# Performance work log

Measured on AMD Instinct MI355X. Metric: run time of the kernel, lower is better.

The kernel has to match this reference:

```python
import jax, jax.numpy as jnp
import numpy as np

EMBED = 1024
HEADS = 16
HEAD_DIM = EMBED // HEADS

def setup_inputs() -> dict:
    key = jax.random.key(0)
    ks = jax.random.split(key, 12)
    N, L, E = 4, 2048, EMBED
    s = 1.0 / np.sqrt(E)
    return {
        "values": jax.random.normal(ks[0], (N, L, E), jnp.float32),
        "keys": jax.random.normal(ks[1], (N, L, E), jnp.float32),
        "query": jax.random.normal(ks[2], (N, L, E), jnp.float32),
        "mask": jnp.ones((N, 1, 1, L), jnp.int32),
        "Wv": jax.random.normal(ks[3], (E, E), jnp.float32) * s,
        "bv": jnp.zeros((E,), jnp.float32),
        "Wk": jax.random.normal(ks[4], (E, E), jnp.float32) * s,
        "bk": jnp.zeros((E,), jnp.float32),
        "Wq": jax.random.normal(ks[5], (E, E), jnp.float32) * s,
        "bq": jnp.zeros((E,), jnp.float32),
        "Wo": jax.random.normal(ks[6], (E, E), jnp.float32) * s,
        "bo": jnp.zeros((E,), jnp.float32),
    }

def reference(values, keys, query, mask, Wv, bv, Wk, bk, Wq, bq, Wo, bo):
    N, L, E = values.shape
    H, D = HEADS, HEAD_DIM
    v = (values @ Wv + bv).reshape(N, L, H, D)
    k = (keys @ Wk + bk).reshape(N, L, H, D)
    q = (query @ Wq + bq).reshape(N, L, H, D)
    # energy: [N, H, Lq, Lk]
    energy = jnp.einsum('nqhd,nkhd->nhqk', q, k)
    energy = jnp.where(mask == 0, jnp.float32(-1e20), energy)
    attn = jax.nn.softmax(energy / np.sqrt(D), axis=3)
    out = jnp.einsum('nhqk,nkhd->nqhd', attn, v).reshape(N, L, E)
    return out @ Wo + bo
```

## Files before the change

### kernel.cpp

```cpp
#include <hip/hip_runtime.h>
#include <hip/hip_bf16.h>


#define N_B 4
#define L_S 2048
#define E_D 1024
#define H_N 16
#define D_H 64

typedef __attribute__((ext_vector_type(8))) short short8;
typedef __attribute__((ext_vector_type(8))) unsigned short ushort8;
typedef __attribute__((ext_vector_type(4))) unsigned short ushort4v;
typedef __attribute__((ext_vector_type(4))) float f32x4;

#define EXP2F(x) __builtin_amdgcn_exp2f(x)

__device__ __forceinline__ unsigned short f2b(float f) {
    unsigned int u = __builtin_bit_cast(unsigned int, f);
    u += 0x7fffu + ((u >> 16) & 1u);
    return (unsigned short)(u >> 16);
}

__device__ __forceinline__ void gload16(const void* g, void* l) {
    __builtin_amdgcn_global_load_lds(
        (const __attribute__((address_space(1))) void*)g,
        (__attribute__((address_space(3))) void*)l, 16, 0, 0);
}

__global__ __launch_bounds__(256) void cvt3_kernel(const float* __restrict__ v,
                                                   const float* __restrict__ k,
                                                   const float* __restrict__ q,
                                                   unsigned short* __restrict__ out) {
    int z = blockIdx.y;
    const float* in = (z == 0) ? v : ((z == 1) ? k : q);
    unsigned short* o = out + (size_t)z * (8u << 20);
    size_t i = (size_t)blockIdx.x * 256 + threadIdx.x;
    const float* p = in + i * 8;
    ushort8 ov;
#pragma unroll
    for (int j = 0; j < 8; j++) ov[j] = f2b(p[j]);
    *(ushort8*)(o + i * 8) = ov;
}

__global__ __launch_bounds__(256) void wtrans4_kernel(const float* __restrict__ W0,
                                                      const float* __restrict__ W1,
                                                      const float* __restrict__ W2,
                                                      const float* __restrict__ W3,
                                                      unsigned short* __restrict__ WtBase) {
    __shared__ float t[64][65];
    int z = blockIdx.z;
    const float* W = (z == 0) ? W0 : ((z == 1) ? W1 : ((z == 2) ? W2 : W3));
    unsigned short* Wt = WtBase + (size_t)z * (1u << 20);
    int bx = blockIdx.x, by = blockIdx.y;
    int tx = threadIdx.x;
    int r0 = tx >> 4;
    int c4 = (tx & 15) << 2;
#pragma unroll
    for (int rr = 0; rr < 64; rr += 16) {
        const float* src = W + (size_t)(by * 64 + rr + r0) * E_D + bx * 64 + c4;
        float4 v = *(const float4*)src;
        t[rr + r0][c4 + 0] = v.x; t[rr + r0][c4 + 1] = v.y;
        t[rr + r0][c4 + 2] = v.z; t[rr + r0][c4 + 3] = v.w;
    }
    __syncthreads();
#pragma unroll
    for (int rr = 0; rr < 64; rr += 16) {
        int nrow = bx * 64 + rr + r0;
        ushort4v o;
#pragma unroll
        for (int j = 0; j < 4; j++) o[j] = f2b(t[c4 + j][rr + r0]);
        *(ushort4v*)(Wt + (size_t)nrow * E_D + by * 64 + c4) = o;
    }
}

template <int OUTF32>
__device__ __forceinline__ void gemm_body(
    const unsigned short* __restrict__ A, const unsigned short* __restrict__ Bt,
    const float* __restrict__ bias, void* __restrict__ C,
    int K, int Nc, float scale,
    unsigned short* As, unsigned short* Bs, int n0, int m0) {
    int lane = threadIdx.x & 63, wave = threadIdx.x >> 6;
    int wr = (wave >> 1) * 64, wc = (wave & 1) * 64;
    f32x4 acc[4][4] = {};
    int nk = K >> 6;
    for (int kt = 0; kt < nk; ++kt) {
#pragma unroll
        for (int i = 0; i < 4; i++) {
            int c = (i * 4 + wave) * 64 + lane;
            int row = c >> 3;
            int csw = (c & 7) ^ (row & 7);
            gload16(A + (size_t)(m0 + row) * K + kt * 64 + csw * 8,
                    As + (size_t)(i * 4 + wave) * 512);
            gload16(Bt + (size_t)(n0 + row) * K + kt * 64 + csw * 8,
                    Bs + (size_t)(i * 4 + wave) * 512);
        }
        __syncthreads();
#pragma unroll
        for (int ks = 0; ks < 2; ++ks) {
            short8 a[4], b[4];
#pragma unroll
            for (int mi = 0; mi < 4; mi++) {
                int row = wr + mi * 16 + (lane & 15);
                int ch = (ks * 4 + (lane >> 4)) ^ (row & 7);
                a[mi] = *(const short8*)(As + row * 64 + ch * 8);
            }
#pragma unroll
            for (int ni = 0; ni < 4; ni++) {
                int col = wc + ni * 16 + (lane & 15);
                int ch = (ks * 4 + (lane >> 4)) ^ (col & 7);
                b[ni] = *(const short8*)(Bs + col * 64 + ch * 8);
            }
#pragma unroll
            for (int mi = 0; mi < 4; mi++)
#pragma unroll
                for (int ni = 0; ni < 4; ni++)
                    acc[mi][ni] = __builtin_amdgcn_mfma_f32_16x16x32_bf16(
                        a[mi], b[ni], acc[mi][ni], 0, 0, 0);
        }
        __syncthreads();
    }
#pragma unroll
    for (int ni = 0; ni < 4; ni++) {
        int col = n0 + wc + ni * 16 + (lane & 15);
        float bb = bias[col];
#pragma unroll
        for (int mi = 0; mi < 4; mi++) {
            int rbase = m0 + wr + mi * 16 + (lane >> 4) * 4;
#pragma unroll
            for (int r = 0; r < 4; r++) {
                float v = (acc[mi][ni][r] + bb) * scale;
                if (OUTF32)
                    ((float*)C)[(size_t)(rbase + r) * Nc + col] = v;
                else
                    ((unsigned short*)C)[(size_t)(rbase + r) * Nc + col] = f2b(v);
            }
        }
    }
}

template <int OUTF32>
__global__ __launch_bounds__(256, 3) void gemm_kernel(
    const unsigned short* __restrict__ A, const unsigned short* __restrict__ Bt,
    const float* __restrict__ bias, void* __restrict__ C,
    int M, int K, int Nc, float scale) {
    __shared__ unsigned short As[128 * 64];
    __shared__ unsigned short Bs[128 * 64];
    gemm_body<OUTF32>(A, Bt, bias, C, K, Nc, scale, As, Bs,
                      blockIdx.x * 128, blockIdx.y * 128);
}

__global__ __launch_bounds__(256, 3) void gemm3_kernel(
    const unsigned short* __restrict__ Abase, const unsigned short* __restrict__ Wtbase,
    const float* __restrict__ bv, const float* __restrict__ bk, const float* __restrict__ bq,
    unsigned short* __restrict__ Cbase, float qscale) {
    __shared__ unsigned short As[128 * 64];
    __shared__ unsigned short Bs[128 * 64];
    int z = blockIdx.z;
    const unsigned short* A  = Abase + (size_t)z * (8u << 20);
    const unsigned short* Bt = Wtbase + (size_t)z * (1u << 20);
    const float* bias = (z == 0) ? bv : ((z == 1) ? bk : bq);
    unsigned short* C = Cbase + (size_t)z * (8u << 20);
    float scale = (z == 2) ? qscale : 1.0f;
    gemm_body<0>(A, Bt, bias, C, E_D, E_D, scale, As, Bs,
                 blockIdx.x * 128, blockIdx.y * 128);
}

__global__ __launch_bounds__(256) void vtrans_kernel(const unsigned short* __restrict__ v,
                                                     unsigned short* __restrict__ vt) {
    __shared__ unsigned short t[64 * 65];
    int l0 = blockIdx.x * 64, h = blockIdx.y, n = blockIdx.z;
    int tx = threadIdx.x;
    int r = tx >> 3;
    int c8 = (tx & 7) << 3;
#pragma unroll
    for (int rr = 0; rr < 64; rr += 32) {
        ushort8 val = *(const ushort8*)(v + (size_t)(n * L_S + l0 + rr + r) * E_D + h * 64 + c8);
#pragma unroll
        for (int j = 0; j < 8; j++) t[(rr + r) * 65 + c8 + j] = val[j];
    }
    __syncthreads();
#pragma unroll
    for (int rr = 0; rr < 64; rr += 32) {
        int d = rr + r;
        ushort8 o;
#pragma unroll
        for (int j = 0; j < 8; j++) o[j] = t[(c8 + j) * 65 + d];
        *(ushort8*)(vt + (size_t)((n * H_N + h) * D_H + d) * L_S + l0 + c8) = o;
    }
}

__global__ __launch_bounds__(256, 3) void attn_kernel(
    const unsigned short* __restrict__ qb, const unsigned short* __restrict__ kb,
    const unsigned short* __restrict__ vt, const int* __restrict__ mask,
    unsigned short* __restrict__ aout) {
    __shared__ unsigned short Ks[2][64 * 64];
    __shared__ unsigned short Vs[2][64 * 64];
    __shared__ unsigned short Ps[4][32 * 64];
    __shared__ alignas(8) unsigned char okb[256];
    int lane = threadIdx.x & 63, wave = threadIdx.x >> 6;
    int g = lane >> 4, c = lane & 15;
    const float SHIFT = 20.0f;

    int bid = blockIdx.x;
    int w = (bid & 7) * 128 + (bid >> 3);
    int q0 = (w & 15) * 128;
    int h = (w >> 4) & 15;
    int n = w >> 8;

    const unsigned short* qptr  = qb + (size_t)n * L_S * E_D + h * 64;
    const unsigned short* kbase = kb + (size_t)n * L_S * E_D + h * 64;
    const unsigned short* vbase = vt + (size_t)(n * H_N + h) * D_H * L_S;
    const int* mbase = mask + n * L_S;

    {
        int t8 = threadIdx.x * 8;
        int4 ma = *(const int4*)(mbase + t8);
        int4 mb = *(const int4*)(mbase + t8 + 4);
        int ok = (ma.x != 0) & (ma.y != 0) & (ma.z != 0) & (ma.w != 0) &
                 (mb.x != 0) & (mb.y != 0) & (mb.z != 0) & (mb.w != 0);
        okb[threadIdx.x] = (unsigned char)ok;
    }
    unsigned short* Qs = &Ps[0][0];
#pragma unroll
    for (int i = 0; i < 4; i++) {
        int cc = (i * 4 + wave) * 64 + lane;
        int row = cc >> 3, csw = (cc & 7) ^ (row & 7);
        gload16(qptr + (size_t)(q0 + row) * E_D + csw * 8, Qs + (i * 4 + wave) * 512);
    }
#pragma unroll
    for (int i = 0; i < 2; i++) {
        int cc = (i * 4 + wave) * 64 + lane;
        int row = cc >> 3, csw = (cc & 7) ^ (row & 7);
        gload16(kbase + (size_t)row * E_D + csw * 8, Ks[0] + (i * 4 + wave) * 512);
        gload16(vbase + (size_t)row * L_S + csw * 8, Vs[0] + (i * 4 + wave) * 512);
    }
    __syncthreads();

    short8 qf[2][2];
#pragma unroll
    for (int m = 0; m < 2; m++)
#pragma unroll
        for (int kd = 0; kd < 2; kd++) {
            int row = wave * 32 + m * 16 + c;
            int ch = (kd * 4 + g) ^ (row & 7);
            qf[m][kd] = *(const short8*)(Qs + row * 64 + ch * 8);
        }

    f32x4 o[2][4] = {};
    float lrun[2] = {0.f, 0.f};
    unsigned short* pw = &Ps[wave][0];

    const int NT = L_S / 64;
    for (int kt = 0; kt < NT; ++kt) {
        int cur = kt & 1;
        if (kt + 1 < NT) {
#pragma unroll
            for (int i = 0; i < 2; i++) {
                int cc = (i * 4 + wave) * 64 + lane;
                int row = cc >> 3, csw = (cc & 7) ^ (row & 7);
                gload16(kbase + (size_t)((kt + 1) * 64 + row) * E_D + csw * 8,
                        Ks[cur ^ 1] + (i * 4 + wave) * 512);
                gload16(vbase + (size_t)row * L_S + (kt + 1) * 64 + csw * 8,
                        Vs[cur ^ 1] + (i * 4 + wave) * 512);
            }
            asm volatile("s_waitcnt vmcnt(4)" ::: "memory");
        } else {
            asm volatile("s_waitcnt vmcnt(0)" ::: "memory");
        }
        __builtin_amdgcn_s_barrier();
        __builtin_amdgcn_sched_barrier(0);

        const unsigned short* KsC = Ks[cur];
        const unsigned short* VsC = Vs[cur];

        f32x4 sT[2][4] = {};
        __builtin_amdgcn_s_setprio(1);
#pragma unroll
        for (int kd = 0; kd < 2; kd++)
#pragma unroll
            for (int kg = 0; kg < 4; kg++) {
                int krow = kg * 16 + c;
                int ch = (kd * 4 + g) ^ (krow & 7);
                short8 kf = *(const short8*)(KsC + krow * 64 + ch * 8);
                sT[0][kg] = __builtin_amdgcn_mfma_f32_16x16x32_bf16(kf, qf[0][kd], sT[0][kg], 0, 0, 0);
                sT[1][kg] = __builtin_amdgcn_mfma_f32_16x16x32_bf16(kf, qf[1][kd], sT[1][kg], 0, 0, 0);
            }
        __builtin_amdgcn_s_setprio(0);

        uint2 fl = *(const uint2*)&okb[kt * 8];
        bool dense = ((fl.x & fl.y) == 0x01010101u);
        if (!dense) {
#pragma unroll
            for (int kg = 0; kg < 4; kg++) {
                int4 mv = *(const int4*)(mbase + kt * 64 + kg * 16 + g * 4);
                float m0 = mv.x ? 0.f : -1e30f;
                float m1 = mv.y ? 0.f : -1e30f;
                float m2 = mv.z ? 0.f : -1e30f;
                float m3 = mv.w ? 0.f : -1e30f;
                sT[0][kg][0] += m0; sT[1][kg][0] += m0;
                sT[0][kg][1] += m1; sT[1][kg][1] += m1;
                sT[0][kg][2] += m2; sT[1][kg][2] += m2;
                sT[0][kg][3] += m3; sT[1][kg][3] += m3;
            }
        }
#pragma unroll
        for (int m = 0; m < 2; m++) {
            float ps = 0.f;
            int prow = m * 16 + c;
#pragma unroll
            for (int kg = 0; kg < 4; kg++) {
                float p0 = EXP2F(sT[m][kg][0] - SHIFT);
                float p1 = EXP2F(sT[m][kg][1] - SHIFT);
                float p2 = EXP2F(sT[m][kg][2] - SHIFT);
                float p3 = EXP2F(sT[m][kg][3] - SHIFT);
                ps += (p0 + p1) + (p2 + p3);
                unsigned int w0, w1;
                asm("v_cvt_pk_bf16_f32 %0, %1, %2" : "=v"(w0) : "v"(p0), "v"(p1));
                asm("v_cvt_pk_bf16_f32 %0, %1, %2" : "=v"(w1) : "v"(p2), "v"(p3));
                int c16 = kg * 2 + (g >> 1);
                int off = prow * 64 + ((c16 ^ (prow & 7)) << 3) + ((g & 1) << 2);
                uint2 wv; wv.x = w0; wv.y = w1;
                *(uint2*)(pw + off) = wv;
            }
            ps += __shfl_xor(ps, 16);
            ps += __shfl_xor(ps, 32);
            lrun[m] += ps;
        }
        __builtin_amdgcn_s_setprio(1);
#pragma unroll
        for (int kk = 0; kk < 2; kk++) {
            short8 pb[2];
#pragma unroll
            for (int m = 0; m < 2; m++) {
                int prow = m * 16 + c;
                int ch = (kk * 4 + g) ^ (prow & 7);
                pb[m] = *(const short8*)(pw + prow * 64 + ch * 8);
            }
#pragma unroll
            for (int dg = 0; dg < 4; dg++) {
                int drow = dg * 16 + c;
                int ch = (kk * 4 + g) ^ (drow & 7);
                short8 vb = *(const short8*)(VsC + drow * 64 + ch * 8);
                o[0][dg] = __builtin_amdgcn_mfma_f32_16x16x32_bf16(vb, pb[0], o[0][dg], 0, 0, 0);
                o[1][dg] = __builtin_amdgcn_mfma_f32_16x16x32_bf16(vb, pb[1], o[1][dg], 0, 0, 0);
            }
        }
        __builtin_amdgcn_s_setprio(0);
        asm volatile("s_waitcnt lgkmcnt(0)" ::: "memory");
        __builtin_amdgcn_s_barrier();
    }
#pragma unroll
    for (int m = 0; m < 2; m++) {
        float inv = 1.f / lrun[m];
        int row = q0 + wave * 32 + m * 16 + c;
#pragma unroll
        for (int dg = 0; dg < 4; dg++) {
            ushort4v ov;
#pragma unroll
            for (int r = 0; r < 4; r++) ov[r] = f2b(o[m][dg][r] * inv);
            *(ushort4v*)(aout + (size_t)(n * L_S + row) * E_D + h * 64 + dg * 16 + g * 4) = ov;
        }
    }
}

extern "C" void kernel_launch(void* const* d_in, const int* in_sizes, int n_in,
                              void* d_out, int out_size, void* d_ws, size_t ws_size,
                              hipStream_t stream) {
    const float* values = (const float*)d_in[0];
    const float* keys   = (const float*)d_in[1];
    const float* query  = (const float*)d_in[2];
    const int*   mask   = (const int*)d_in[3];
    const float* Wv = (const float*)d_in[4];  const float* bv = (const float*)d_in[5];
    const float* Wk = (const float*)d_in[6];  const float* bk = (const float*)d_in[7];
    const float* Wq = (const float*)d_in[8];  const float* bq = (const float*)d_in[9];
    const float* Wo = (const float*)d_in[10]; const float* bo = (const float*)d_in[11];
    float* out = (float*)d_out;
    char* ws = (char*)d_ws;
    const size_t MB = 1ull << 20;
    unsigned short* xv  = (unsigned short*)(ws + 0 * MB);
    unsigned short* wtv = (unsigned short*)(ws + 48 * MB);
    unsigned short* wto = (unsigned short*)(ws + 54 * MB);
    unsigned short* vbf = (unsigned short*)(ws + 56 * MB);
    unsigned short* kbf = (unsigned short*)(ws + 72 * MB);
    unsigned short* qbf = (unsigned short*)(ws + 88 * MB);
    unsigned short* vT  = (unsigned short*)(ws + 0 * MB);
    unsigned short* aob = (unsigned short*)(ws + 16 * MB);

    const float QS = 0.125f * 1.4426950408889634f;

    cvt3_kernel<<<dim3(4096, 3), 256, 0, stream>>>(values, keys, query, xv);
    wtrans4_kernel<<<dim3(16, 16, 4), 256, 0, stream>>>(Wv, Wk, Wq, Wo, wtv);
    gemm3_kernel<<<dim3(E_D / 128, (N_B * L_S) / 128, 3), 256, 0, stream>>>(
        xv, wtv, bv, bk, bq, vbf, QS);
    vtrans_kernel<<<dim3(32, 16, 4), 256, 0, stream>>>(vbf, vT);
    attn_kernel<<<dim3(1024), 256, 0, stream>>>(qbf, kbf, vT, mask, aob);
    gemm_kernel<1><<<dim3(E_D / 128, (N_B * L_S) / 128), 256, 0, stream>>>(
        aob, wto, bo, out, N_B * L_S, E_D, E_D, 1.0f);
}
```

Baseline: 229.9 us.

## Double attention query tile to 256 rows with 8 waves sharing K/V tiles

The attention kernel now launches 512 blocks of 512 threads. Each block handles 256 query rows with eight waves, so every K/V tile loaded into LDS is reused by twice as many query rows and total K/V traffic is halved. The block-to-(batch, head, query-tile) mapping is rearranged so that blocks sharing a head land on the same XCD. The costs are a larger Ps buffer in LDS, half as many blocks (fewer in flight on the device), and a larger barrier group per tile.

```diff
diff --git a/kernel.cpp b/kernel.cpp
--- a/kernel.cpp
+++ b/kernel.cpp
@@ -189,30 +189,31 @@
     }
 }
 
-__global__ __launch_bounds__(256, 3) void attn_kernel(
+__global__ __launch_bounds__(512, 4) void attn_kernel(
     const unsigned short* __restrict__ qb, const unsigned short* __restrict__ kb,
     const unsigned short* __restrict__ vt, const int* __restrict__ mask,
     unsigned short* __restrict__ aout) {
     __shared__ unsigned short Ks[2][64 * 64];
     __shared__ unsigned short Vs[2][64 * 64];
-    __shared__ unsigned short Ps[4][32 * 64];
+    __shared__ unsigned short Ps[8][32 * 64];
     __shared__ alignas(8) unsigned char okb[256];
     int lane = threadIdx.x & 63, wave = threadIdx.x >> 6;
     int g = lane >> 4, c = lane & 15;
     const float SHIFT = 20.0f;
 
     int bid = blockIdx.x;
-    int w = (bid & 7) * 128 + (bid >> 3);
-    int q0 = (w & 15) * 128;
-    int h = (w >> 4) & 15;
-    int n = w >> 8;
+    int xcd = bid & 7, idx = bid >> 3;
+    int grp = xcd * 8 + (idx >> 3);
+    int q0 = (idx & 7) * 256;
+    int h = grp & 15;
+    int n = grp >> 4;
 
     const unsigned short* qptr  = qb + (size_t)n * L_S * E_D + h * 64;
     const unsigned short* kbase = kb + (size_t)n * L_S * E_D + h * 64;
     const unsigned short* vbase = vt + (size_t)(n * H_N + h) * D_H * L_S;
     const int* mbase = mask + n * L_S;
 
-    {
+    if (threadIdx.x < 256) {
         int t8 = threadIdx.x * 8;
         int4 ma = *(const int4*)(mbase + t8);
         int4 mb = *(const int4*)(mbase + t8 + 4);
@@ -223,16 +224,16 @@
     unsigned short* Qs = &Ps[0][0];
 #pragma unroll
     for (int i = 0; i < 4; i++) {
-        int cc = (i * 4 + wave) * 64 + lane;
+        int ci = i * 8 + wave;
+        int cc = ci * 64 + lane;
         int row = cc >> 3, csw = (cc & 7) ^ (row & 7);
-        gload16(qptr + (size_t)(q0 + row) * E_D + csw * 8, Qs + (i * 4 + wave) * 512);
-    }
-#pragma unroll
-    for (int i = 0; i < 2; i++) {
-        int cc = (i * 4 + wave) * 64 + lane;
+        gload16(qptr + (size_t)(q0 + row) * E_D + csw * 8, Qs + (size_t)ci * 512);
+    }
+    {
+        int cc = wave * 64 + lane;
         int row = cc >> 3, csw = (cc & 7) ^ (row & 7);
-        gload16(kbase + (size_t)row * E_D + csw * 8, Ks[0] + (i * 4 + wave) * 512);
-        gload16(vbase + (size_t)row * L_S + csw * 8, Vs[0] + (i * 4 + wave) * 512);
+        gload16(kbase + (size_t)row * E_D + csw * 8, Ks[0] + wave * 512);
+        gload16(vbase + (size_t)row * L_S + csw * 8, Vs[0] + wave * 512);
     }
     __syncthreads();
 
@@ -254,16 +255,13 @@
     for (int kt = 0; kt < NT; ++kt) {
         int cur = kt & 1;
         if (kt + 1 < NT) {
-#pragma unroll
-            for (int i = 0; i < 2; i++) {
-                int cc = (i * 4 + wave) * 64 + lane;
-                int row = cc >> 3, csw = (cc & 7) ^ (row & 7);
-                gload16(kbase + (size_t)((kt + 1) * 64 + row) * E_D + csw * 8,
-                        Ks[cur ^ 1] + (i * 4 + wave) * 512);
-                gload16(vbase + (size_t)row * L_S + (kt + 1) * 64 + csw * 8,
-                        Vs[cur ^ 1] + (i * 4 + wave) * 512);
-            }
-            asm volatile("s_waitcnt vmcnt(4)" ::: "memory");
+            int cc = wave * 64 + lane;
+            int row = cc >> 3, csw = (cc & 7) ^ (row & 7);
+            gload16(kbase + (size_t)((kt + 1) * 64 + row) * E_D + csw * 8,
+                    Ks[cur ^ 1] + wave * 512);
+            gload16(vbase + (size_t)row * L_S + (kt + 1) * 64 + csw * 8,
+                    Vs[cur ^ 1] + wave * 512);
+            asm volatile("s_waitcnt vmcnt(2)" ::: "memory");
         } else {
             asm volatile("s_waitcnt vmcnt(0)" ::: "memory");
         }
@@ -393,7 +391,7 @@
     gemm3_kernel<<<dim3(E_D / 128, (N_B * L_S) / 128, 3), 256, 0, stream>>>(
         xv, wtv, bv, bk, bq, vbf, QS);
     vtrans_kernel<<<dim3(32, 16, 4), 256, 0, stream>>>(vbf, vT);
-    attn_kernel<<<dim3(1024), 256, 0, stream>>>(qbf, kbf, vT, mask, aob);
+    attn_kernel<<<dim3(512), 512, 0, stream>>>(qbf, kbf, vT, mask, aob);
     gemm_kernel<1><<<dim3(E_D / 128, (N_B * L_S) / 128), 256, 0, stream>>>(
         aob, wto, bo, out, N_B * L_S, E_D, E_D, 1.0f);
 }
```

After: 217.8 us. -5.3%, faster.
